# Performance work log

Measured on AMD Instinct MI355X. Metric: run time of the kernel, lower is better.

## Reference

```python
import jax, jax.numpy as jnp
import numpy as np

N, S, D, d, H = 8, 2048, 256, 128, 10  # H = rel_k_heights
SCALING = float(np.sqrt(2 * d))


def _ln(x, g, b):
    m = jnp.mean(x, axis=-1, keepdims=True)
    v = jnp.var(x, axis=-1, keepdims=True)
    return (x - m) / jnp.sqrt(v + 1e-5) * g + b


def setup_inputs() -> dict:
    key = jax.random.key(0)
    ks = jax.random.split(key, 12)
    std = 0.02
    p = lambda k, shape: (jax.random.normal(k, shape, jnp.float32) * std)
    return {
        'sequence': jax.random.normal(ks[0], (N, S, D), jnp.float32),
        'attention_mask': jax.random.bernoulli(ks[1], 0.9, (N, S, S)),
        'heights': jax.random.randint(ks[2], (N, S), 0, 50),
        'W_init': p(ks[3], (D, D)), 'b_init': jnp.zeros((D,), jnp.float32),
        'ln_g': jnp.ones((D,), jnp.float32), 'ln_b': jnp.zeros((D,), jnp.float32),
        'W_U': p(ks[4], (D, 2 * D)), 'b_U': jnp.zeros((2 * D,), jnp.float32),
        'W_V': p(ks[5], (D, 2 * D)), 'b_V': jnp.zeros((2 * D,), jnp.float32),
        'W_Z': p(ks[6], (D, d)), 'b_Z': jnp.zeros((d,), jnp.float32),
        'os_gamma': p(ks[7], (3, d)),  # torch inits gamma ~ N(0, 0.02)
        'os_beta': jnp.zeros((3, d), jnp.float32),
        'embed_heights': jax.random.normal(ks[8], (H, d), jnp.float32),
        'W_out': p(ks[9], (2 * D, D)), 'b_out': jnp.zeros((D,), jnp.float32),
        'W_gate': p(ks[10], (2 * D, D)), 'b_gate': jnp.zeros((D,), jnp.float32),
    }


def reference(sequence, attention_mask, heights,
              W_init, b_init, ln_g, ln_b,
              W_U, b_U, W_V, b_V, W_Z, b_Z,
              os_gamma, os_beta, embed_heights,
              W_out, b_out, W_gate, b_gate):
    S0 = (S - 1) // 2  # 1023
    mask = attention_mask[:, :S0, S0:]          # [N,S0,S1]
    res = sequence

    x = _ln(sequence @ W_init + b_init, ln_g, ln_b)            # [N,S,D]
    U = jax.nn.silu(x[:, :S0, :] @ W_U + b_U)                  # [N,S0,2D]
    Z = jax.nn.silu(x @ W_Z + b_Z)                             # [N,S,d]
    V = jax.nn.silu(x[:, S0:, :] @ W_V + b_V)                  # [N,S1,2D]

    # OffsetScale: Q, Qp, K from Z
    Q = (Z * os_gamma[0] + os_beta[0])[:, :S0, :]              # [N,S0,d]
    Qp = (Z * os_gamma[1] + os_beta[1])[:, :S0, :]             # [N,S0,d]
    K = (Z * os_gamma[2] + os_beta[2])[:, S0:, :]              # [N,S1,d]

    energy = jnp.einsum('bsd,btd->bst', Q, K)                  # [N,S0,S1]

    # relative-height bias: direct gather (math-equivalent to one-hot*sum)
    Q_h = jnp.einsum('bsd,hd->bsh', Qp, embed_heights)         # [N,S0,H]
    rel = heights[:, None, S0:] - heights[:, :S0, None]        # [N,S0,S1]
    rel_idx = jnp.clip(rel, 1, H) - 1
    rel_energy = jnp.take_along_axis(Q_h, rel_idx, axis=2)     # [N,S0,S1]

    logits = (energy + rel_energy) / SCALING
    logits = jnp.where(mask, logits, -9999.0)
    attn = jax.nn.softmax(logits, axis=-1)                     # [N,S0,S1]

    V_ = jnp.einsum('bst,btd->bsd', attn, V)                   # [N,S0,2D]
    out = (U * V_) @ W_out + b_out                             # [N,S0,D]
    gates = jax.nn.sigmoid(
        jnp.concatenate([out, res[:, :S0, :]], axis=-1) @ W_gate + b_gate)
    out = gates * out + (1.0 - gates) * res[:, :S0, :]
    out = jnp.concatenate([out, res[:, S0:, :]], axis=1)       # [N,S,D]
    return out
```

## Files before the change

### kernel.cpp

```cpp
#include <hip/hip_runtime.h>
#include <cstdint>
#include <cstddef>

#define S_TOT 2048
#define S0_   1023
#define S1_   1025
#define D_    256
#define D2_   512
#define DZ_   128
#define NB_   8
#define NT_   17
#define KT16_ 68
#define SCALE_INV (1.0f/16.0f)
#define XPAD  264
#define UPAD  520
#define NTILES (NB_*S0_*NT_)
#define MP_BLOCKS ((NTILES + 15)/16)

typedef __attribute__((ext_vector_type(8))) short short8v;
typedef __attribute__((ext_vector_type(4))) short short4v;
typedef __attribute__((ext_vector_type(4))) float f32x4;
typedef unsigned long long u64;

__device__ __forceinline__ short f2bf(float f){
  unsigned u = __float_as_uint(f);
  unsigned r = (u + 0x7FFFu + ((u >> 16) & 1u)) >> 16;
  return (short)r;
}
__device__ __forceinline__ float bf2f(short s){
  return __uint_as_float(((unsigned)(unsigned short)s) << 16);
}
__device__ __forceinline__ float silu_f(float x){ return x / (1.f + __expf(-x)); }

__device__ __forceinline__ short8v load_afrag(const short* arow, int kt, int khi){
  short4v lo = *reinterpret_cast<const short4v*>(arow + kt*32 + khi);
  short4v hi = *reinterpret_cast<const short4v*>(arow + kt*32 + khi + 16);
  short8v r = {lo[0],lo[1],lo[2],lo[3],hi[0],hi[1],hi[2],hi[3]};
  return r;
}

__global__ __launch_bounds__(256) void k_prep(
    const float* __restrict__ W_init, const float* __restrict__ W_U,
    const float* __restrict__ W_V,    const float* __restrict__ W_Z,
    const float* __restrict__ W_out,  const float* __restrict__ W_gate,
    short* __restrict__ WpI, short* __restrict__ WpU, short* __restrict__ WpV,
    short* __restrict__ WpZ, short* __restrict__ WpO, short* __restrict__ WpG,
    const unsigned char* __restrict__ amask, u64* __restrict__ maskb)
{
  const int blk = blockIdx.x;
  if (blk < 304){
    const float* W; short* dst; int K, N, base;
    if      (blk <  32){ W=W_init; dst=WpI; K=256; N=256; base=0;   }
    else if (blk <  96){ W=W_U;    dst=WpU; K=256; N=512; base=32;  }
    else if (blk < 160){ W=W_V;    dst=WpV; K=256; N=512; base=96;  }
    else if (blk < 176){ W=W_Z;    dst=WpZ; K=256; N=128; base=160; }
    else if (blk < 240){ W=W_out;  dst=WpO; K=512; N=256; base=176; }
    else               { W=W_gate; dst=WpG; K=512; N=256; base=240; }
    const int wv = threadIdx.x >> 6, lane = threadIdx.x & 63;
    const int KT = K >> 5;
    const int tile = (blk - base)*4 + wv;
    const int nt = tile / KT, kt = tile - nt*KT;
    const int n = nt*16 + (lane & 15);
    const int kbase = kt*32 + ((lane>>4)<<2);
    short8v v;
    #pragma unroll
    for (int j=0;j<8;++j){
      int k = kbase + (j&3) + ((j>>2)<<4);
      v[j] = f2bf(W[(size_t)k*N + n]);
    }
    *reinterpret_cast<short8v*>(dst + ((size_t)tile*64 + lane)*8) = v;
  } else {
    const int lane = threadIdx.x & 63;
    const int g0 = ((blk - 304)*4 + (threadIdx.x >> 6))*4;
    #pragma unroll
    for (int j=0;j<4;++j){
      int tg = g0 + j;
      if (tg >= NTILES) break;
      int row = tg / NT_;
      int t   = tg - row*NT_;
      int b   = row / S0_;
      int q   = row - b*S0_;
      int key = t*64 + lane;
      unsigned char v = 0;
      if (key < S1_) v = amask[((size_t)(b*S_TOT + q))*S_TOT + S0_ + key];
      u64 bits = __ballot(v != 0);
      if (lane == 0) maskb[tg] = bits;
    }
  }
}

__global__ __launch_bounds__(256) void k_x(
    const float* __restrict__ seq, const short* __restrict__ Wp,
    const float* __restrict__ b_init,
    const float* __restrict__ ln_g, const float* __restrict__ ln_b,
    short* __restrict__ xb, float* __restrict__ out)
{
  __shared__ short s_a[64*XPAD];
  const int tid = threadIdx.x, lane = tid & 63, wv = tid >> 6;
  const int R0 = blockIdx.x * 64;
  const int colb = lane & 15, khi = (lane>>4)<<2;

  for (int c = tid; c < 64*64; c += 256){
    int row = c >> 6, c4 = (c & 63) << 2;
    int g = R0 + row;
    float4 f = *reinterpret_cast<const float4*>(seq + (size_t)g*D_ + c4);
    short4v h = { f2bf(f.x), f2bf(f.y), f2bf(f.z), f2bf(f.w) };
    *reinterpret_cast<short4v*>(&s_a[row*XPAD + c4]) = h;
    if ((g & 2047) >= S0_)
      *reinterpret_cast<float4*>(out + (size_t)g*D_ + c4) = f;
  }
  __syncthreads();

  f32x4 acc[16];
  #pragma unroll
  for (int nt=0;nt<16;++nt) acc[nt] = (f32x4){0.f,0.f,0.f,0.f};

  const short* arow = &s_a[(wv*16 + colb)*XPAD];
  #pragma unroll
  for (int kt=0; kt<8; ++kt){
    short8v a = load_afrag(arow, kt, khi);
    #pragma unroll
    for (int nt=0; nt<16; ++nt){
      short8v b = *reinterpret_cast<const short8v*>(Wp + ((size_t)(nt*8 + kt)*64 + lane)*8);
      acc[nt] = __builtin_amdgcn_mfma_f32_16x16x32_bf16(a, b, acc[nt], 0, 0, 0);
    }
  }

  float sum[4] = {0.f,0.f,0.f,0.f};
  #pragma unroll
  for (int nt=0; nt<16; ++nt){
    float bv = b_init[nt*16 + colb];
    #pragma unroll
    for (int r=0;r<4;++r){ acc[nt][r] += bv; sum[r] += acc[nt][r]; }
  }
  #pragma unroll
  for (int r=0;r<4;++r){
    #pragma unroll
    for (int m=1;m<16;m<<=1) sum[r] += __shfl_xor(sum[r], m, 64);
    sum[r] *= (1.f/256.f);
  }
  float var[4] = {0.f,0.f,0.f,0.f};
  #pragma unroll
  for (int nt=0; nt<16; ++nt)
    #pragma unroll
    for (int r=0;r<4;++r){ float d = acc[nt][r]-sum[r]; var[r] += d*d; }
  #pragma unroll
  for (int r=0;r<4;++r){
    #pragma unroll
    for (int m=1;m<16;m<<=1) var[r] += __shfl_xor(var[r], m, 64);
    var[r] = rsqrtf(var[r]*(1.f/256.f) + 1e-5f);
  }
  #pragma unroll
  for (int nt=0; nt<16; ++nt){
    int col = nt*16 + colb;
    float g = ln_g[col], bb = ln_b[col];
    #pragma unroll
    for (int r=0;r<4;++r){
      float xn = (acc[nt][r]-sum[r])*var[r]*g + bb;
      s_a[(wv*16 + ((lane>>4)<<2) + r)*XPAD + col] = f2bf(xn);
    }
  }
  __syncthreads();
  for (int c = tid; c < 64*32; c += 256){
    int row = c >> 5, c8 = (c & 31) << 3;
    *reinterpret_cast<short8v*>(xb + (size_t)(R0+row)*D_ + c8) =
        *reinterpret_cast<const short8v*>(&s_a[row*XPAD + c8]);
  }
}

__global__ __launch_bounds__(256) void k_gemmZV(
    const short* __restrict__ xb,
    const short* __restrict__ WpZ, const float* __restrict__ b_Z,
    short* __restrict__ Zb,
    const short* __restrict__ WpV, const float* __restrict__ b_V,
    short* __restrict__ VtF)
{
  __shared__ short s_a[64*XPAD];
  __shared__ short s_t[64][72];
  const int blk = blockIdx.x;
  const int tid = threadIdx.x, lane = tid & 63, wv = tid >> 6;
  const int wy = wv >> 1, wx = wv & 1;
  const int colb = lane & 15, khi = (lane>>4)<<2;

  if (blk < 512){
    const int R0 = (blk >> 1) * 64;
    const int C0 = (blk & 1) * 64;

    for (int c = tid; c < 64*32; c += 256){
      int r = c >> 5, c8 = (c & 31) << 3;
      size_t xrow = (size_t)(R0 + r);
      *reinterpret_cast<short8v*>(&s_a[r*XPAD + c8]) =
          *reinterpret_cast<const short8v*>(xb + xrow*D_ + c8);
    }
    __syncthreads();

    f32x4 acc[2][2];
    #pragma unroll
    for(int i=0;i<2;++i)
      #pragma unroll
      for(int j=0;j<2;++j) acc[i][j] = (f32x4){0.f,0.f,0.f,0.f};

    const short* ar0 = &s_a[(wy*32 + colb)*XPAD];
    const short* ar1 = ar0 + 16*XPAD;
    const int ntg = (C0 >> 4) + wx*2;
    #pragma unroll
    for (int kt=0; kt<8; ++kt){
      short8v a0 = load_afrag(ar0, kt, khi);
      short8v a1 = load_afrag(ar1, kt, khi);
      short8v b0 = *reinterpret_cast<const short8v*>(WpZ + ((size_t)((ntg+0)*8 + kt)*64 + lane)*8);
      short8v b1 = *reinterpret_cast<const short8v*>(WpZ + ((size_t)((ntg+1)*8 + kt)*64 + lane)*8);
      acc[0][0] = __builtin_amdgcn_mfma_f32_16x16x32_bf16(a0, b0, acc[0][0], 0,0,0);
      acc[0][1] = __builtin_amdgcn_mfma_f32_16x16x32_bf16(a0, b1, acc[0][1], 0,0,0);
      acc[1][0] = __builtin_amdgcn_mfma_f32_16x16x32_bf16(a1, b0, acc[1][0], 0,0,0);
      acc[1][1] = __builtin_amdgcn_mfma_f32_16x16x32_bf16(a1, b1, acc[1][1], 0,0,0);
    }
    #pragma unroll
    for (int sj=0; sj<2; ++sj){
      int col = C0 + wx*32 + sj*16 + colb;
      float bv = b_Z[col];
      #pragma unroll
      for (int si=0; si<2; ++si){
        #pragma unroll
        for (int r=0;r<4;++r){
          int orow = R0 + wy*32 + si*16 + ((lane>>4)<<2) + r;
          Zb[(size_t)orow*DZ_ + col] = f2bf(silu_f(acc[si][sj][r] + bv));
        }
      }
    }
  } else {
    const int idx = blk - 512;
    const int t   = idx % 17;
    const int rest= idx / 17;
    const int C0  = (rest & 7) * 64;
    const int b   = rest >> 3;
    const int R0  = t * 64;

    for (int c = tid; c < 64*32; c += 256){
      int r = c >> 5, c8 = (c & 31) << 3;
      int k = R0 + r; if (k > 1024) k = 1024;
      size_t xrow = (size_t)b*S_TOT + S0_ + k;
      *reinterpret_cast<short8v*>(&s_a[r*XPAD + c8]) =
          *reinterpret_cast<const short8v*>(xb + xrow*D_ + c8);
    }
    __syncthreads();

    f32x4 acc[2][2];
    #pragma unroll
    for(int i=0;i<2;++i)
      #pragma unroll
      for(int j=0;j<2;++j) acc[i][j] = (f32x4){0.f,0.f,0.f,0.f};

    const short* ar0 = &s_a[(wy*32 + colb)*XPAD];
    const short* ar1 = ar0 + 16*XPAD;
    const int ntg = (C0 >> 4) + wx*2;
    #pragma unroll
    for (int kt=0; kt<8; ++kt){
      short8v a0 = load_afrag(ar0, kt, khi);
      short8v a1 = load_afrag(ar1, kt, khi);
      short8v b0 = *reinterpret_cast<const short8v*>(WpV + ((size_t)((ntg+0)*8 + kt)*64 + lane)*8);
      short8v b1 = *reinterpret_cast<const short8v*>(WpV + ((size_t)((ntg+1)*8 + kt)*64 + lane)*8);
      acc[0][0] = __builtin_amdgcn_mfma_f32_16x16x32_bf16(a0, b0, acc[0][0], 0,0,0);
      acc[0][1] = __builtin_amdgcn_mfma_f32_16x16x32_bf16(a0, b1, acc[0][1], 0,0,0);
      acc[1][0] = __builtin_amdgcn_mfma_f32_16x16x32_bf16(a1, b0, acc[1][0], 0,0,0);
      acc[1][1] = __builtin_amdgcn_mfma_f32_16x16x32_bf16(a1, b1, acc[1][1], 0,0,0);
    }
    #pragma unroll
    for (int sj=0; sj<2; ++sj){
      int cl = wx*32 + sj*16 + colb;
      float bv = b_V[C0 + cl];
      #pragma unroll
      for (int si=0; si<2; ++si){
        #pragma unroll
        for (int r=0;r<4;++r){
          int rl = wy*32 + si*16 + ((lane>>4)<<2) + r;
          s_t[cl][rl] = f2bf(silu_f(acc[si][sj][r] + bv));
        }
      }
    }
    __syncthreads();
    {
      const int vt_l = tid >> 6;
      const int vloc = vt_l*16 + (lane & 15);
      const int krow = (lane>>4)<<2;
      #pragma unroll
      for (int kt=0; kt<2; ++kt){
        short8v f;
        #pragma unroll
        for (int j=0;j<8;++j){
          int kl = kt*32 + krow + (j&3) + ((j>>2)<<4);
          short v = s_t[vloc][kl];
          if (R0 + kl >= S1_) v = 0;
          f[j] = v;
        }
        size_t o = (((size_t)b*32 + (C0>>4) + vt_l)*(2*NT_) + 2*t + kt)*64 + lane;
        *reinterpret_cast<short8v*>(VtF + o*8) = f;
      }
    }
  }
}

__global__ __launch_bounds__(256) void k_packZ(const short* __restrict__ Zb,
                                               short* __restrict__ ZkF){
  const int lane = threadIdx.x & 63;
  const int w = blockIdx.x*4 + (threadIdx.x >> 6);
  if (w >= NB_*KT16_*4) return;
  const int b = w / (KT16_*4);
  const int rem = w - b*(KT16_*4);
  const int kt16 = rem >> 2, kt = rem & 3;
  int key = kt16*16 + (lane & 15); if (key > 1024) key = 1024;
  const short* zr = Zb + ((size_t)(b*S_TOT + S0_ + key))*DZ_ + kt*32 + ((lane>>4)<<2);
  short4v lo = *reinterpret_cast<const short4v*>(zr);
  short4v hi = *reinterpret_cast<const short4v*>(zr + 16);
  short8v f = {lo[0],lo[1],lo[2],lo[3],hi[0],hi[1],hi[2],hi[3]};
  *reinterpret_cast<short8v*>(ZkF + ((size_t)w*64 + lane)*8) = f;
}

#define SMEM_BYTES 51712
__global__ __launch_bounds__(256,2) void k_flash(
    const short* __restrict__ Zb, const short* __restrict__ ZkF,
    const short* __restrict__ VtF, const u64* __restrict__ maskb,
    const short* __restrict__ xb,
    const short* __restrict__ WpU, const float* __restrict__ b_U,
    const short* __restrict__ Wpo, const float* __restrict__ b_out,
    const short* __restrict__ Wpg, const float* __restrict__ b_gate,
    const float* __restrict__ seq, float* __restrict__ out,
    const int* __restrict__ heights,
    const float* __restrict__ os_g, const float* __restrict__ os_b,
    const float* __restrict__ embH)
{
  __shared__ __align__(16) char smem[SMEM_BYTES];
  __shared__ float  s_qh[16][12];
  __shared__ float  s_qb[16];
  __shared__ int    s_hk[NT_*64];
  __shared__ u64    s_mb[16][NT_];
  __shared__ float  s_mx[4][16];
  __shared__ float  s_sm[4][16];

  short8v (*s_pl)[64] = reinterpret_cast<short8v(*)[64]>(smem);
  short8v (*s_ph)[64] = reinterpret_cast<short8v(*)[64]>(smem + 17408);
  short   (*s_qg)[132] = reinterpret_cast<short(*)[132]>(smem);
  short* sUV = reinterpret_cast<short*>(smem);
  short* sO  = reinterpret_cast<short*>(smem + 16640);
  short* sX  = reinterpret_cast<short*>(smem + 34816);
  short* sR  = reinterpret_cast<short*>(smem + 43264);

  const int tid = threadIdx.x, lane = tid & 63, wv = tid >> 6;
  const int b  = blockIdx.x & 7;
  const int qt = blockIdx.x >> 3;
  const int q0 = qt * 16;

  for (int c = tid; c < 16*32; c += 256){
    int r = c >> 5, c8 = (c & 31) << 3;
    int q = min(q0 + r, S0_-1);
    *reinterpret_cast<short8v*>(&sX[r*XPAD + c8]) =
        *reinterpret_cast<const short8v*>(xb + ((size_t)(b*S_TOT + q))*D_ + c8);
  }
  for (int c = tid; c < 16*64; c += 256){
    int r = c >> 6, c4 = (c & 63) << 2;
    int q = min(q0 + r, S0_-1);
    float4 f = *reinterpret_cast<const float4*>(seq + ((size_t)(b*S_TOT + q))*D_ + c4);
    short4v h = { f2bf(f.x), f2bf(f.y), f2bf(f.z), f2bf(f.w) };
    *reinterpret_cast<short4v*>(&sR[r*XPAD + c4]) = h;
  }

  {
    int row = tid >> 4, part = tid & 15;
    int q = q0 + row; if (q > S0_-1) q = S0_-1;
    const short* zrow = Zb + ((size_t)(b*S_TOT + q))*DZ_ + part*8;
    float qb_acc = 0.f;
    float qh_acc[10];
    #pragma unroll
    for (int h=0;h<10;++h) qh_acc[h] = 0.f;
    #pragma unroll
    for (int e=0; e<8; ++e){
      int dz = part*8 + e;
      float z = bf2f(zrow[e]);
      float Q  = z*os_g[dz]      + os_b[dz];
      float Qp = z*os_g[DZ_+dz]  + os_b[DZ_+dz];
      s_qg[row][dz] = f2bf(Q * os_g[2*DZ_+dz]);
      qb_acc += Q * os_b[2*DZ_+dz];
      #pragma unroll
      for (int h=0;h<10;++h) qh_acc[h] += Qp * embH[h*DZ_ + dz];
    }
    #pragma unroll
    for (int m=1;m<16;m<<=1){
      qb_acc += __shfl_xor(qb_acc, m, 64);
      #pragma unroll
      for (int h=0;h<10;++h) qh_acc[h] += __shfl_xor(qh_acc[h], m, 64);
    }
    if (part == 0){
      s_qb[row] = qb_acc;
      #pragma unroll
      for (int h=0;h<10;++h) s_qh[row][h] = qh_acc[h];
    }
  }
  for (int k = tid; k < NT_*64; k += 256)
    s_hk[k] = (k < S1_) ? heights[b*S_TOT + S0_ + k] : 0;
  for (int idx = tid; idx < 16*NT_; idx += 256){
    int qq = idx / NT_, tt = idx - qq*NT_;
    int qr = q0 + qq; if (qr > S0_-1) qr = S0_-1;
    s_mb[qq][tt] = maskb[((size_t)(b*S0_ + qr))*NT_ + tt];
  }
  __syncthreads();

  const int qcol = lane & 15, khi = (lane>>4)<<2;
  int qme = q0 + qcol; if (qme > S0_-1) qme = S0_-1;
  const int hq = heights[b*S_TOT + qme];
  const float qb = s_qb[qcol];

  short8v qgf[4];
  #pragma unroll
  for (int kt=0; kt<4; ++kt) qgf[kt] = load_afrag(&s_qg[qcol][0], kt, khi);

  f32x4 sc[5][4];
  float tmw = -1e30f;
  #pragma unroll
  for (int it=0; it<5; ++it){
    const int t = it*4 + wv;
    if (t < NT_){
      u64 mb = s_mb[qcol][t];
      #pragma unroll
      for (int st=0; st<4; ++st){
        f32x4 c = (f32x4){0.f,0.f,0.f,0.f};
        #pragma unroll
        for (int kt=0; kt<4; ++kt){
          short8v a = *reinterpret_cast<const short8v*>(
              ZkF + (((size_t)(b*KT16_ + t*4 + st)*4 + kt)*64 + lane)*8);
          c = __builtin_amdgcn_mfma_f32_16x16x32_bf16(a, qgf[kt], c, 0,0,0);
        }
        int4 hk4 = *reinterpret_cast<const int4*>(&s_hk[t*64 + st*16 + khi]);
        #pragma unroll
        for (int r=0;r<4;++r){
          int hk = (&hk4.x)[r];
          int idx = min(max(hk - hq, 1), 10) - 1;
          float v = (c[r] + qb + s_qh[qcol][idx]) * SCALE_INV;
          int kl = st*16 + khi + r;
          v = ((mb >> kl) & 1ull) ? v : -9999.f;
          c[r] = v;
          tmw = fmaxf(tmw, v);
        }
        sc[it][st] = c;
      }
    }
  }
  tmw = fmaxf(tmw, __shfl_xor(tmw, 16, 64));
  tmw = fmaxf(tmw, __shfl_xor(tmw, 32, 64));
  if (lane < 16) s_mx[wv][lane] = tmw;
  __syncthreads();

  const float m = fmaxf(fmaxf(s_mx[0][qcol], s_mx[1][qcol]),
                        fmaxf(s_mx[2][qcol], s_mx[3][qcol]));
  float ls = 0.f;
  #pragma unroll
  for (int it=0; it<5; ++it){
    const int t = it*4 + wv;
    if (t < NT_){
      #pragma unroll
      for (int st=0; st<4; ++st)
        #pragma unroll
        for (int r=0;r<4;++r){
          float p = __expf(sc[it][st][r] - m);
          ls += p;
          sc[it][st][r] = p;
        }
      short8v pa0, pa1;
      #pragma unroll
      for (int j=0;j<8;++j){
        pa0[j] = f2bf(sc[it][(j>>2)][j&3]);
        pa1[j] = f2bf(sc[it][2 + (j>>2)][j&3]);
      }
      s_pl[t][lane] = pa0;
      s_ph[t][lane] = pa1;
    }
  }
  ls += __shfl_xor(ls, 16, 64);
  ls += __shfl_xor(ls, 32, 64);
  if (lane < 16) s_sm[wv][lane] = ls;
  __syncthreads();

  float lrow[4];
  #pragma unroll
  for (int r=0;r<4;++r){
    int qr = khi + r;
    lrow[r] = s_sm[0][qr] + s_sm[1][qr] + s_sm[2][qr] + s_sm[3][qr];
  }
  f32x4 O[8];
  #pragma unroll
  for (int vt=0; vt<8; ++vt) O[vt] = (f32x4){0.f,0.f,0.f,0.f};
  for (int t=0; t<NT_; ++t){
    short8v pa0 = s_pl[t][lane];
    short8v pa1 = s_ph[t][lane];
    #pragma unroll
    for (int vt=0; vt<8; ++vt){
      size_t vb = ((size_t)b*32 + wv*8 + vt)*(2*NT_) + 2*t;
      short8v b0 = *reinterpret_cast<const short8v*>(VtF + (vb*64 + lane)*8);
      short8v b1 = *reinterpret_cast<const short8v*>(VtF + ((vb+1)*64 + lane)*8);
      O[vt] = __builtin_amdgcn_mfma_f32_16x16x32_bf16(pa0, b0, O[vt], 0,0,0);
      O[vt] = __builtin_amdgcn_mfma_f32_16x16x32_bf16(pa1, b1, O[vt], 0,0,0);
    }
  }
  __syncthreads();

  f32x4 accu[8];
  #pragma unroll
  for (int vt=0; vt<8; ++vt) accu[vt] = (f32x4){0.f,0.f,0.f,0.f};
  {
    const short* xrow = &sX[qcol*XPAD];
    #pragma unroll
    for (int kt=0; kt<8; ++kt){
      short8v a = load_afrag(xrow, kt, khi);
      #pragma unroll
      for (int vt=0; vt<8; ++vt){
        int nt = wv*8 + vt;
        short8v bw = *reinterpret_cast<const short8v*>(WpU + ((size_t)(nt*8 + kt)*64 + lane)*8);
        accu[vt] = __builtin_amdgcn_mfma_f32_16x16x32_bf16(a, bw, accu[vt], 0,0,0);
      }
    }
  }
  float inv[4];
  #pragma unroll
  for (int r=0;r<4;++r) inv[r] = 1.f / lrow[r];
  #pragma unroll
  for (int vt=0; vt<8; ++vt){
    int v = wv*128 + vt*16 + qcol;
    float bu = b_U[v];
    #pragma unroll
    for (int r=0;r<4;++r){
      float u = silu_f(accu[vt][r] + bu);
      sUV[(khi + r)*UPAD + v] = f2bf(u * O[vt][r] * inv[r]);
    }
  }
  __syncthreads();

  f32x4 acc_o[4];
  #pragma unroll
  for (int j=0;j<4;++j) acc_o[j] = (f32x4){0.f,0.f,0.f,0.f};
  {
    const short* arow = &sUV[qcol*UPAD];
    #pragma unroll
    for (int kt=0; kt<16; ++kt){
      short8v a = load_afrag(arow, kt, khi);
      #pragma unroll
      for (int j=0;j<4;++j){
        int nt = wv*4 + j;
        short8v bw = *reinterpret_cast<const short8v*>(Wpo + ((size_t)(nt*16 + kt)*64 + lane)*8);
        acc_o[j] = __builtin_amdgcn_mfma_f32_16x16x32_bf16(a, bw, acc_o[j], 0,0,0);
      }
    }
  }
  #pragma unroll
  for (int j=0;j<4;++j){
    int col = (wv*4+j)*16 + qcol;
    float bv = b_out[col];
    #pragma unroll
    for (int r=0;r<4;++r){
      acc_o[j][r] += bv;
      sO[(khi + r)*XPAD + col] = f2bf(acc_o[j][r]);
    }
  }
  __syncthreads();

  f32x4 acc_g[4];
  #pragma unroll
  for (int j=0;j<4;++j) acc_g[j] = (f32x4){0.f,0.f,0.f,0.f};
  {
    const short* orow_p = &sO[qcol*XPAD];
    const short* rrow_p = &sR[qcol*XPAD];
    #pragma unroll
    for (int kt=0; kt<8; ++kt){
      short8v a = load_afrag(orow_p, kt, khi);
      #pragma unroll
      for (int j=0;j<4;++j){
        int nt = wv*4 + j;
        short8v bw = *reinterpret_cast<const short8v*>(Wpg + ((size_t)(nt*16 + kt)*64 + lane)*8);
        acc_g[j] = __builtin_amdgcn_mfma_f32_16x16x32_bf16(a, bw, acc_g[j], 0,0,0);
      }
    }
    #pragma unroll
    for (int kt=0; kt<8; ++kt){
      short8v a = load_afrag(rrow_p, kt, khi);
      #pragma unroll
      for (int j=0;j<4;++j){
        int nt = wv*4 + j;
        short8v bw = *reinterpret_cast<const short8v*>(Wpg + ((size_t)(nt*16 + 8 + kt)*64 + lane)*8);
        acc_g[j] = __builtin_amdgcn_mfma_f32_16x16x32_bf16(a, bw, acc_g[j], 0,0,0);
      }
    }
  }
  #pragma unroll
  for (int j=0;j<4;++j){
    int col = (wv*4+j)*16 + qcol;
    float bg = b_gate[col];
    #pragma unroll
    for (int r=0;r<4;++r){
      int q = q0 + khi + r;
      if (q < S0_){
        float res = seq[((size_t)(b*S_TOT + q))*D_ + col];
        float g = 1.f/(1.f + __expf(-(acc_g[j][r] + bg)));
        out[((size_t)(b*S_TOT + q))*D_ + col] = g*acc_o[j][r] + (1.f-g)*res;
      }
    }
  }
}

extern "C" void kernel_launch(void* const* d_in, const int* in_sizes, int n_in,
                              void* d_out, int out_size, void* d_ws, size_t ws_size,
                              hipStream_t stream)
{
  const float* seq    = (const float*)d_in[0];
  const unsigned char* amask = (const unsigned char*)d_in[1];
  const int*   heights= (const int*)d_in[2];
  const float* W_init = (const float*)d_in[3];
  const float* b_init = (const float*)d_in[4];
  const float* ln_g   = (const float*)d_in[5];
  const float* ln_b   = (const float*)d_in[6];
  const float* W_U    = (const float*)d_in[7];
  const float* b_U    = (const float*)d_in[8];
  const float* W_V    = (const float*)d_in[9];
  const float* b_V    = (const float*)d_in[10];
  const float* W_Z    = (const float*)d_in[11];
  const float* b_Z    = (const float*)d_in[12];
  const float* os_g   = (const float*)d_in[13];
  const float* os_b   = (const float*)d_in[14];
  const float* embH   = (const float*)d_in[15];
  const float* W_out  = (const float*)d_in[16];
  const float* b_out  = (const float*)d_in[17];
  const float* W_gate = (const float*)d_in[18];
  const float* b_gate = (const float*)d_in[19];
  float* out = (float*)d_out;

  char* w = (char*)d_ws;
  short* Zb  = (short*)w;                w += (size_t)16512*128*2;
  short* VtF = (short*)w;                w += (size_t)8*32*(2*NT_)*64*8*2;
  short* ZkF = (short*)w;                w += (size_t)NB_*KT16_*4*64*8*2;
  short* xb  = (short*)w;                w += (size_t)16384*256*2;
  u64*  maskb = (u64*)w;                 w += (size_t)NB_*S0_*NT_*8;
  short* WpI = (short*)w;                w += (size_t)65536*2;
  short* WpU = (short*)w;                w += (size_t)131072*2;
  short* WpV = (short*)w;                w += (size_t)131072*2;
  short* WpZ = (short*)w;                w += (size_t)32768*2;
  short* WpO = (short*)w;                w += (size_t)131072*2;
  short* WpG = (short*)w;                w += (size_t)131072*2;

  hipLaunchKernelGGL(k_prep, dim3(304 + MP_BLOCKS), dim3(256), 0, stream,
      W_init, W_U, W_V, W_Z, W_out, W_gate,
      WpI, WpU, WpV, WpZ, WpO, WpG, amask, maskb);

  hipLaunchKernelGGL(k_x, dim3(256), dim3(256), 0, stream,
      seq, WpI, b_init, ln_g, ln_b, xb, out);

  hipLaunchKernelGGL(k_gemmZV, dim3(512 + 1088), dim3(256), 0, stream,
      xb, WpZ, b_Z, Zb, WpV, b_V, VtF);

  hipLaunchKernelGGL(k_packZ, dim3((NB_*KT16_*4 + 3)/4), dim3(256), 0, stream, Zb, ZkF);

  hipLaunchKernelGGL(k_flash, dim3(512), dim3(256), 0, stream,
      Zb, ZkF, VtF, maskb, xb, WpU, b_U, WpO, b_out, WpG, b_gate,
      seq, out, heights, os_g, os_b, embH);
}
```

Before: 109.8 us.

## Process two 16-query tiles per 512-thread flash block to share K/V loads

Each attention block now covers 32 queries as two 16-row tiles, run by 8 waves instead of 4. Every K fragment from ZkF, V fragment from VtF and weight fragment from WpU, Wpo and Wpg is loaded once and fed to two MFMAs, one per tile. This roughly halves global and cache traffic per query in the score, PV and epilogue GEMMs. The cost is about twice the LDS (around 103 KB) and twice the accumulator registers, and only 256 blocks are launched. That likely limits residency to one block per CU and reduces latency hiding.

```diff
diff --git a/kernel.cpp b/kernel.cpp
--- a/kernel.cpp
+++ b/kernel.cpp
@@ -315,8 +315,8 @@
   *reinterpret_cast<short8v*>(ZkF + ((size_t)w*64 + lane)*8) = f;
 }
 
-#define SMEM_BYTES 51712
-__global__ __launch_bounds__(256,2) void k_flash(
+#define SMEM_BYTES 103424
+__global__ __launch_bounds__(512,2) void k_flash(
     const short* __restrict__ Zb, const short* __restrict__ ZkF,
     const short* __restrict__ VtF, const u64* __restrict__ maskb,
     const short* __restrict__ xb,
@@ -329,33 +329,35 @@
     const float* __restrict__ embH)
 {
   __shared__ __align__(16) char smem[SMEM_BYTES];
-  __shared__ float  s_qh[16][12];
-  __shared__ float  s_qb[16];
+  __shared__ float  s_qh[32][12];
+  __shared__ float  s_qb[32];
   __shared__ int    s_hk[NT_*64];
-  __shared__ u64    s_mb[16][NT_];
-  __shared__ float  s_mx[4][16];
-  __shared__ float  s_sm[4][16];
-
-  short8v (*s_pl)[64] = reinterpret_cast<short8v(*)[64]>(smem);
-  short8v (*s_ph)[64] = reinterpret_cast<short8v(*)[64]>(smem + 17408);
-  short   (*s_qg)[132] = reinterpret_cast<short(*)[132]>(smem);
+  __shared__ u64    s_mb[32][NT_];
+  __shared__ float  s_mxA[8][16], s_mxB[8][16];
+  __shared__ float  s_smA[8][16], s_smB[8][16];
+
+  short8v (*s_pAl)[64] = reinterpret_cast<short8v(*)[64]>(smem);
+  short8v (*s_pAh)[64] = reinterpret_cast<short8v(*)[64]>(smem + 17408);
+  short8v (*s_pBl)[64] = reinterpret_cast<short8v(*)[64]>(smem + 34816);
+  short8v (*s_pBh)[64] = reinterpret_cast<short8v(*)[64]>(smem + 52224);
+  short   (*s_qg)[132] = reinterpret_cast<short(*)[132]>(smem + 34816);
   short* sUV = reinterpret_cast<short*>(smem);
-  short* sO  = reinterpret_cast<short*>(smem + 16640);
-  short* sX  = reinterpret_cast<short*>(smem + 34816);
-  short* sR  = reinterpret_cast<short*>(smem + 43264);
+  short* sO  = reinterpret_cast<short*>(smem + 34816);
+  short* sX  = reinterpret_cast<short*>(smem + 69632);
+  short* sR  = reinterpret_cast<short*>(smem + 86528);
 
   const int tid = threadIdx.x, lane = tid & 63, wv = tid >> 6;
   const int b  = blockIdx.x & 7;
-  const int qt = blockIdx.x >> 3;
-  const int q0 = qt * 16;
-
-  for (int c = tid; c < 16*32; c += 256){
+  const int qp = blockIdx.x >> 3;
+  const int q0 = qp * 32;
+
+  for (int c = tid; c < 32*32; c += 512){
     int r = c >> 5, c8 = (c & 31) << 3;
     int q = min(q0 + r, S0_-1);
     *reinterpret_cast<short8v*>(&sX[r*XPAD + c8]) =
         *reinterpret_cast<const short8v*>(xb + ((size_t)(b*S_TOT + q))*D_ + c8);
   }
-  for (int c = tid; c < 16*64; c += 256){
+  for (int c = tid; c < 32*64; c += 512){
     int r = c >> 6, c4 = (c & 63) << 2;
     int q = min(q0 + r, S0_-1);
     float4 f = *reinterpret_cast<const float4*>(seq + ((size_t)(b*S_TOT + q))*D_ + c4);
@@ -394,210 +396,250 @@
       for (int h=0;h<10;++h) s_qh[row][h] = qh_acc[h];
     }
   }
-  for (int k = tid; k < NT_*64; k += 256)
+  for (int k = tid; k < NT_*64; k += 512)
     s_hk[k] = (k < S1_) ? heights[b*S_TOT + S0_ + k] : 0;
-  for (int idx = tid; idx < 16*NT_; idx += 256){
+  for (int idx = tid; idx < 32*NT_; idx += 512){
     int qq = idx / NT_, tt = idx - qq*NT_;
-    int qr = q0 + qq; if (qr > S0_-1) qr = S0_-1;
+    int qr = min(q0 + qq, S0_-1);
     s_mb[qq][tt] = maskb[((size_t)(b*S0_ + qr))*NT_ + tt];
   }
   __syncthreads();
 
   const int qcol = lane & 15, khi = (lane>>4)<<2;
-  int qme = q0 + qcol; if (qme > S0_-1) qme = S0_-1;
-  const int hq = heights[b*S_TOT + qme];
-  const float qb = s_qb[qcol];
-
-  short8v qgf[4];
-  #pragma unroll
-  for (int kt=0; kt<4; ++kt) qgf[kt] = load_afrag(&s_qg[qcol][0], kt, khi);
-
-  f32x4 sc[5][4];
-  float tmw = -1e30f;
-  #pragma unroll
-  for (int it=0; it<5; ++it){
-    const int t = it*4 + wv;
+  const int hqA = heights[b*S_TOT + min(q0 + qcol,      S0_-1)];
+  const int hqB = heights[b*S_TOT + min(q0 + 16 + qcol, S0_-1)];
+  const float qbA = s_qb[qcol], qbB = s_qb[16 + qcol];
+
+  short8v qgfA[4], qgfB[4];
+  #pragma unroll
+  for (int kt=0; kt<4; ++kt){
+    qgfA[kt] = load_afrag(&s_qg[qcol][0],      kt, khi);
+    qgfB[kt] = load_afrag(&s_qg[16 + qcol][0], kt, khi);
+  }
+
+  f32x4 scA[3][4], scB[3][4];
+  float tmA = -1e30f, tmB = -1e30f;
+  #pragma unroll
+  for (int it=0; it<3; ++it){
+    const int t = it*8 + wv;
     if (t < NT_){
-      u64 mb = s_mb[qcol][t];
+      u64 mbA = s_mb[qcol][t], mbB = s_mb[16 + qcol][t];
       #pragma unroll
       for (int st=0; st<4; ++st){
-        f32x4 c = (f32x4){0.f,0.f,0.f,0.f};
+        f32x4 cA = (f32x4){0.f,0.f,0.f,0.f};
+        f32x4 cB = (f32x4){0.f,0.f,0.f,0.f};
         #pragma unroll
         for (int kt=0; kt<4; ++kt){
           short8v a = *reinterpret_cast<const short8v*>(
               ZkF + (((size_t)(b*KT16_ + t*4 + st)*4 + kt)*64 + lane)*8);
-          c = __builtin_amdgcn_mfma_f32_16x16x32_bf16(a, qgf[kt], c, 0,0,0);
+          cA = __builtin_amdgcn_mfma_f32_16x16x32_bf16(a, qgfA[kt], cA, 0,0,0);
+          cB = __builtin_amdgcn_mfma_f32_16x16x32_bf16(a, qgfB[kt], cB, 0,0,0);
         }
         int4 hk4 = *reinterpret_cast<const int4*>(&s_hk[t*64 + st*16 + khi]);
         #pragma unroll
         for (int r=0;r<4;++r){
           int hk = (&hk4.x)[r];
-          int idx = min(max(hk - hq, 1), 10) - 1;
-          float v = (c[r] + qb + s_qh[qcol][idx]) * SCALE_INV;
           int kl = st*16 + khi + r;
-          v = ((mb >> kl) & 1ull) ? v : -9999.f;
-          c[r] = v;
-          tmw = fmaxf(tmw, v);
+          int iA = min(max(hk - hqA, 1), 10) - 1;
+          float vA = (cA[r] + qbA + s_qh[qcol][iA]) * SCALE_INV;
+          vA = ((mbA >> kl) & 1ull) ? vA : -9999.f;
+          cA[r] = vA; tmA = fmaxf(tmA, vA);
+          int iB = min(max(hk - hqB, 1), 10) - 1;
+          float vB = (cB[r] + qbB + s_qh[16 + qcol][iB]) * SCALE_INV;
+          vB = ((mbB >> kl) & 1ull) ? vB : -9999.f;
+          cB[r] = vB; tmB = fmaxf(tmB, vB);
         }
-        sc[it][st] = c;
-      }
-    }
-  }
-  tmw = fmaxf(tmw, __shfl_xor(tmw, 16, 64));
-  tmw = fmaxf(tmw, __shfl_xor(tmw, 32, 64));
-  if (lane < 16) s_mx[wv][lane] = tmw;
+        scA[it][st] = cA; scB[it][st] = cB;
+      }
+    }
+  }
+  tmA = fmaxf(tmA, __shfl_xor(tmA, 16, 64));
+  tmA = fmaxf(tmA, __shfl_xor(tmA, 32, 64));
+  tmB = fmaxf(tmB, __shfl_xor(tmB, 16, 64));
+  tmB = fmaxf(tmB, __shfl_xor(tmB, 32, 64));
+  if (lane < 16){ s_mxA[wv][lane] = tmA; s_mxB[wv][lane] = tmB; }
   __syncthreads();
 
-  const float m = fmaxf(fmaxf(s_mx[0][qcol], s_mx[1][qcol]),
-                        fmaxf(s_mx[2][qcol], s_mx[3][qcol]));
-  float ls = 0.f;
-  #pragma unroll
-  for (int it=0; it<5; ++it){
-    const int t = it*4 + wv;
+  float mA = -1e30f, mB = -1e30f;
+  #pragma unroll
+  for (int w=0; w<8; ++w){
+    mA = fmaxf(mA, s_mxA[w][qcol]);
+    mB = fmaxf(mB, s_mxB[w][qcol]);
+  }
+  float lsA = 0.f, lsB = 0.f;
+  #pragma unroll
+  for (int it=0; it<3; ++it){
+    const int t = it*8 + wv;
     if (t < NT_){
       #pragma unroll
       for (int st=0; st<4; ++st)
         #pragma unroll
         for (int r=0;r<4;++r){
-          float p = __expf(sc[it][st][r] - m);
-          ls += p;
-          sc[it][st][r] = p;
+          float pA = __expf(scA[it][st][r] - mA); lsA += pA; scA[it][st][r] = pA;
+          float pB = __expf(scB[it][st][r] - mB); lsB += pB; scB[it][st][r] = pB;
         }
-      short8v pa0, pa1;
+      short8v a0, a1, b0, b1;
       #pragma unroll
       for (int j=0;j<8;++j){
-        pa0[j] = f2bf(sc[it][(j>>2)][j&3]);
-        pa1[j] = f2bf(sc[it][2 + (j>>2)][j&3]);
-      }
-      s_pl[t][lane] = pa0;
-      s_ph[t][lane] = pa1;
-    }
-  }
-  ls += __shfl_xor(ls, 16, 64);
-  ls += __shfl_xor(ls, 32, 64);
-  if (lane < 16) s_sm[wv][lane] = ls;
+        a0[j] = f2bf(scA[it][(j>>2)][j&3]);
+        a1[j] = f2bf(scA[it][2 + (j>>2)][j&3]);
+        b0[j] = f2bf(scB[it][(j>>2)][j&3]);
+        b1[j] = f2bf(scB[it][2 + (j>>2)][j&3]);
+      }
+      s_pAl[t][lane] = a0; s_pAh[t][lane] = a1;
+      s_pBl[t][lane] = b0; s_pBh[t][lane] = b1;
+    }
+  }
+  lsA += __shfl_xor(lsA, 16, 64); lsA += __shfl_xor(lsA, 32, 64);
+  lsB += __shfl_xor(lsB, 16, 64); lsB += __shfl_xor(lsB, 32, 64);
+  if (lane < 16){ s_smA[wv][lane] = lsA; s_smB[wv][lane] = lsB; }
   __syncthreads();
 
-  float lrow[4];
+  float lrA[4], lrB[4];
   #pragma unroll
   for (int r=0;r<4;++r){
     int qr = khi + r;
-    lrow[r] = s_sm[0][qr] + s_sm[1][qr] + s_sm[2][qr] + s_sm[3][qr];
-  }
-  f32x4 O[8];
-  #pragma unroll
-  for (int vt=0; vt<8; ++vt) O[vt] = (f32x4){0.f,0.f,0.f,0.f};
+    float sa = 0.f, sb = 0.f;
+    #pragma unroll
+    for (int w=0; w<8; ++w){ sa += s_smA[w][qr]; sb += s_smB[w][qr]; }
+    lrA[r] = sa; lrB[r] = sb;
+  }
+  f32x4 OA[4], OB[4];
+  #pragma unroll
+  for (int j=0;j<4;++j){ OA[j] = (f32x4){0.f,0.f,0.f,0.f}; OB[j] = (f32x4){0.f,0.f,0.f,0.f}; }
   for (int t=0; t<NT_; ++t){
-    short8v pa0 = s_pl[t][lane];
-    short8v pa1 = s_ph[t][lane];
-    #pragma unroll
-    for (int vt=0; vt<8; ++vt){
-      size_t vb = ((size_t)b*32 + wv*8 + vt)*(2*NT_) + 2*t;
-      short8v b0 = *reinterpret_cast<const short8v*>(VtF + (vb*64 + lane)*8);
-      short8v b1 = *reinterpret_cast<const short8v*>(VtF + ((vb+1)*64 + lane)*8);
-      O[vt] = __builtin_amdgcn_mfma_f32_16x16x32_bf16(pa0, b0, O[vt], 0,0,0);
-      O[vt] = __builtin_amdgcn_mfma_f32_16x16x32_bf16(pa1, b1, O[vt], 0,0,0);
+    short8v pa0 = s_pAl[t][lane], pa1 = s_pAh[t][lane];
+    short8v pb0 = s_pBl[t][lane], pb1 = s_pBh[t][lane];
+    #pragma unroll
+    for (int j=0;j<4;++j){
+      size_t vb = ((size_t)b*32 + wv*4 + j)*(2*NT_) + 2*t;
+      short8v v0 = *reinterpret_cast<const short8v*>(VtF + (vb*64 + lane)*8);
+      short8v v1 = *reinterpret_cast<const short8v*>(VtF + ((vb+1)*64 + lane)*8);
+      OA[j] = __builtin_amdgcn_mfma_f32_16x16x32_bf16(pa0, v0, OA[j], 0,0,0);
+      OA[j] = __builtin_amdgcn_mfma_f32_16x16x32_bf16(pa1, v1, OA[j], 0,0,0);
+      OB[j] = __builtin_amdgcn_mfma_f32_16x16x32_bf16(pb0, v0, OB[j], 0,0,0);
+      OB[j] = __builtin_amdgcn_mfma_f32_16x16x32_bf16(pb1, v1, OB[j], 0,0,0);
     }
   }
   __syncthreads();
 
-  f32x4 accu[8];
-  #pragma unroll
-  for (int vt=0; vt<8; ++vt) accu[vt] = (f32x4){0.f,0.f,0.f,0.f};
+  f32x4 auA[4], auB[4];
+  #pragma unroll
+  for (int j=0;j<4;++j){ auA[j] = (f32x4){0.f,0.f,0.f,0.f}; auB[j] = (f32x4){0.f,0.f,0.f,0.f}; }
   {
-    const short* xrow = &sX[qcol*XPAD];
+    const short* xrA = &sX[qcol*XPAD];
+    const short* xrB = &sX[(16 + qcol)*XPAD];
     #pragma unroll
     for (int kt=0; kt<8; ++kt){
-      short8v a = load_afrag(xrow, kt, khi);
-      #pragma unroll
-      for (int vt=0; vt<8; ++vt){
-        int nt = wv*8 + vt;
-        short8v bw = *reinterpret_cast<const short8v*>(WpU + ((size_t)(nt*8 + kt)*64 + lane)*8);
-        accu[vt] = __builtin_amdgcn_mfma_f32_16x16x32_bf16(a, bw, accu[vt], 0,0,0);
-      }
-    }
-  }
-  float inv[4];
-  #pragma unroll
-  for (int r=0;r<4;++r) inv[r] = 1.f / lrow[r];
-  #pragma unroll
-  for (int vt=0; vt<8; ++vt){
-    int v = wv*128 + vt*16 + qcol;
-    float bu = b_U[v];
-    #pragma unroll
-    for (int r=0;r<4;++r){
-      float u = silu_f(accu[vt][r] + bu);
-      sUV[(khi + r)*UPAD + v] = f2bf(u * O[vt][r] * inv[r]);
-    }
-  }
-  __syncthreads();
-
-  f32x4 acc_o[4];
-  #pragma unroll
-  for (int j=0;j<4;++j) acc_o[j] = (f32x4){0.f,0.f,0.f,0.f};
-  {
-    const short* arow = &sUV[qcol*UPAD];
-    #pragma unroll
-    for (int kt=0; kt<16; ++kt){
-      short8v a = load_afrag(arow, kt, khi);
+      short8v aA = load_afrag(xrA, kt, khi);
+      short8v aB = load_afrag(xrB, kt, khi);
       #pragma unroll
       for (int j=0;j<4;++j){
         int nt = wv*4 + j;
+        short8v bw = *reinterpret_cast<const short8v*>(WpU + ((size_t)(nt*8 + kt)*64 + lane)*8);
+        auA[j] = __builtin_amdgcn_mfma_f32_16x16x32_bf16(aA, bw, auA[j], 0,0,0);
+        auB[j] = __builtin_amdgcn_mfma_f32_16x16x32_bf16(aB, bw, auB[j], 0,0,0);
+      }
+    }
+  }
+  float invA[4], invB[4];
+  #pragma unroll
+  for (int r=0;r<4;++r){ invA[r] = 1.f / lrA[r]; invB[r] = 1.f / lrB[r]; }
+  #pragma unroll
+  for (int j=0;j<4;++j){
+    int v = wv*64 + j*16 + qcol;
+    float bu = b_U[v];
+    #pragma unroll
+    for (int r=0;r<4;++r){
+      float uA = silu_f(auA[j][r] + bu);
+      sUV[(khi + r)*UPAD + v] = f2bf(uA * OA[j][r] * invA[r]);
+      float uB = silu_f(auB[j][r] + bu);
+      sUV[(16 + khi + r)*UPAD + v] = f2bf(uB * OB[j][r] * invB[r]);
+    }
+  }
+  __syncthreads();
+
+  f32x4 aoA[2], aoB[2];
+  #pragma unroll
+  for (int j=0;j<2;++j){ aoA[j] = (f32x4){0.f,0.f,0.f,0.f}; aoB[j] = (f32x4){0.f,0.f,0.f,0.f}; }
+  {
+    const short* uvA = &sUV[qcol*UPAD];
+    const short* uvB = &sUV[(16 + qcol)*UPAD];
+    #pragma unroll
+    for (int kt=0; kt<16; ++kt){
+      short8v aA = load_afrag(uvA, kt, khi);
+      short8v aB = load_afrag(uvB, kt, khi);
+      #pragma unroll
+      for (int j=0;j<2;++j){
+        int nt = wv*2 + j;
         short8v bw = *reinterpret_cast<const short8v*>(Wpo + ((size_t)(nt*16 + kt)*64 + lane)*8);
-        acc_o[j] = __builtin_amdgcn_mfma_f32_16x16x32_bf16(a, bw, acc_o[j], 0,0,0);
-      }
-    }
-  }
-  #pragma unroll
-  for (int j=0;j<4;++j){
-    int col = (wv*4+j)*16 + qcol;
+        aoA[j] = __builtin_amdgcn_mfma_f32_16x16x32_bf16(aA, bw, aoA[j], 0,0,0);
+        aoB[j] = __builtin_amdgcn_mfma_f32_16x16x32_bf16(aB, bw, aoB[j], 0,0,0);
+      }
+    }
+  }
+  #pragma unroll
+  for (int j=0;j<2;++j){
+    int col = (wv*2+j)*16 + qcol;
     float bv = b_out[col];
     #pragma unroll
     for (int r=0;r<4;++r){
-      acc_o[j][r] += bv;
-      sO[(khi + r)*XPAD + col] = f2bf(acc_o[j][r]);
+      aoA[j][r] += bv;  sO[(khi + r)*XPAD + col]      = f2bf(aoA[j][r]);
+      aoB[j][r] += bv;  sO[(16 + khi + r)*XPAD + col] = f2bf(aoB[j][r]);
     }
   }
   __syncthreads();
 
-  f32x4 acc_g[4];
-  #pragma unroll
-  for (int j=0;j<4;++j) acc_g[j] = (f32x4){0.f,0.f,0.f,0.f};
+  f32x4 agA[2], agB[2];
+  #pragma unroll
+  for (int j=0;j<2;++j){ agA[j] = (f32x4){0.f,0.f,0.f,0.f}; agB[j] = (f32x4){0.f,0.f,0.f,0.f}; }
   {
-    const short* orow_p = &sO[qcol*XPAD];
-    const short* rrow_p = &sR[qcol*XPAD];
+    const short* oA = &sO[qcol*XPAD];
+    const short* oB = &sO[(16 + qcol)*XPAD];
+    const short* rA = &sR[qcol*XPAD];
+    const short* rB = &sR[(16 + qcol)*XPAD];
     #pragma unroll
     for (int kt=0; kt<8; ++kt){
-      short8v a = load_afrag(orow_p, kt, khi);
-      #pragma unroll
-      for (int j=0;j<4;++j){
-        int nt = wv*4 + j;
+      short8v aA = load_afrag(oA, kt, khi);
+      short8v aB = load_afrag(oB, kt, khi);
+      #pragma unroll
+      for (int j=0;j<2;++j){
+        int nt = wv*2 + j;
         short8v bw = *reinterpret_cast<const short8v*>(Wpg + ((size_t)(nt*16 + kt)*64 + lane)*8);
-        acc_g[j] = __builtin_amdgcn_mfma_f32_16x16x32_bf16(a, bw, acc_g[j], 0,0,0);
+        agA[j] = __builtin_amdgcn_mfma_f32_16x16x32_bf16(aA, bw, agA[j], 0,0,0);
+        agB[j] = __builtin_amdgcn_mfma_f32_16x16x32_bf16(aB, bw, agB[j], 0,0,0);
       }
     }
     #pragma unroll
     for (int kt=0; kt<8; ++kt){
-      short8v a = load_afrag(rrow_p, kt, khi);
-      #pragma unroll
-      for (int j=0;j<4;++j){
-        int nt = wv*4 + j;
+      short8v aA = load_afrag(rA, kt, khi);
+      short8v aB = load_afrag(rB, kt, khi);
+      #pragma unroll
+      for (int j=0;j<2;++j){
+        int nt = wv*2 + j;
         short8v bw = *reinterpret_cast<const short8v*>(Wpg + ((size_t)(nt*16 + 8 + kt)*64 + lane)*8);
-        acc_g[j] = __builtin_amdgcn_mfma_f32_16x16x32_bf16(a, bw, acc_g[j], 0,0,0);
-      }
-    }
-  }
-  #pragma unroll
-  for (int j=0;j<4;++j){
-    int col = (wv*4+j)*16 + qcol;
+        agA[j] = __builtin_amdgcn_mfma_f32_16x16x32_bf16(aA, bw, agA[j], 0,0,0);
+        agB[j] = __builtin_amdgcn_mfma_f32_16x16x32_bf16(aB, bw, agB[j], 0,0,0);
+      }
+    }
+  }
+  #pragma unroll
+  for (int j=0;j<2;++j){
+    int col = (wv*2+j)*16 + qcol;
     float bg = b_gate[col];
     #pragma unroll
     for (int r=0;r<4;++r){
-      int q = q0 + khi + r;
-      if (q < S0_){
-        float res = seq[((size_t)(b*S_TOT + q))*D_ + col];
-        float g = 1.f/(1.f + __expf(-(acc_g[j][r] + bg)));
-        out[((size_t)(b*S_TOT + q))*D_ + col] = g*acc_o[j][r] + (1.f-g)*res;
+      int qA = q0 + khi + r;
+      if (qA < S0_){
+        float res = seq[((size_t)(b*S_TOT + qA))*D_ + col];
+        float g = 1.f/(1.f + __expf(-(agA[j][r] + bg)));
+        out[((size_t)(b*S_TOT + qA))*D_ + col] = g*aoA[j][r] + (1.f-g)*res;
+      }
+      int qB = q0 + 16 + khi + r;
+      if (qB < S0_){
+        float res = seq[((size_t)(b*S_TOT + qB))*D_ + col];
+        float g = 1.f/(1.f + __expf(-(agB[j][r] + bg)));
+        out[((size_t)(b*S_TOT + qB))*D_ + col] = g*aoB[j][r] + (1.f-g)*res;
       }
     }
   }
@@ -654,7 +696,7 @@
 
   hipLaunchKernelGGL(k_packZ, dim3((NB_*KT16_*4 + 3)/4), dim3(256), 0, stream, Zb, ZkF);
 
-  hipLaunchKernelGGL(k_flash, dim3(512), dim3(256), 0, stream,
+  hipLaunchKernelGGL(k_flash, dim3(256), dim3(512), 0, stream,
       Zb, ZkF, VtF, maskb, xb, WpU, b_U, WpO, b_out, WpG, b_gate,
       seq, out, heights, os_g, os_b, embH);
 }
```

After: 97.77 us (median of 2 runs). -11.0%, faster.
